# Kernel tuning notes

Hardware: AMD Instinct MI355X
Metric: run time of the kernel (lower is better)

The kernel has to match this reference:

```python
import jax, jax.numpy as jnp
import numpy as np

B, N, D, E, C, R = 4, 4096, 2048, 8, 2, 128
K = N * C // E  # tokens routed to each adapter (capacity) = 1024


def setup_inputs() -> dict:
    key = jax.random.key(0)
    ks = jax.random.split(key, 6)
    sc = lambda k, shape, s: (jax.random.normal(k, shape, jnp.float32) * s)
    return {
        "x": sc(ks[0], (B, N, D), 1.0),
        "residual": sc(ks[1], (B, N, D), 1.0),
        "Wg": sc(ks[2], (D, E), 1.0 / np.sqrt(D)),
        "bg": jnp.zeros((E,), jnp.float32),
        "Wd": sc(ks[3], (E, D, R), 1.0 / np.sqrt(D)),
        "bd": jnp.zeros((E, R), jnp.float32),
        "Wu": sc(ks[4], (E, R, D), 1.0 / np.sqrt(R)),
        "bu": jnp.zeros((E, D), jnp.float32),
    }


def reference(x, residual, Wg, bg, Wd, bd, Wu, bu):
    # Gate logits. NOTE: the original code's `nn.Softmax(X).dim` IS the raw
    # logits tensor, so top-k runs on UN-softmaxed logits (faithful quirk).
    logits = x @ Wg + bg                                   # [B,N,E]
    G, I = jax.lax.top_k(jnp.swapaxes(logits, 1, 2), K)    # [B,E,K] each

    # Dispatch: gather top-k tokens per adapter (== one-hot einsum in source).
    X_in = jnp.take_along_axis(x[:, None, :, :], I[..., None], axis=2)  # [B,E,K,D]

    # Per-adapter bottleneck MLP with residual (Adapter: up(relu(down(x))) + x).
    h = jax.nn.relu(jnp.einsum('bekd,edr->bekr', X_in, Wd) + bd[None, :, None, :])
    up = jnp.einsum('bekr,erd->bekd', h, Wu) + bu[None, :, None, :]
    X_e = up + X_in                                        # [B,E,K,D]

    # Weighted scatter-combine back to token positions (== one-hot einsum).
    contrib = (G[..., None] * X_e).reshape(B, E * K, D)
    idx = I.reshape(B, E * K)
    combine = jax.vmap(lambda i, v: jnp.zeros((N, D), x.dtype).at[i].add(v))(idx, contrib)
    return combine + residual
```

## Files before the change

kernel.cpp:

```cpp
#include <hip/hip_runtime.h>

#define B_ 4
#define N_ 4096
#define D_ 2048
#define E_ 8
#define R_ 128
#define K_ 1024

typedef __attribute__((ext_vector_type(8))) short bf16x8;
typedef __attribute__((ext_vector_type(4))) float f32x4;

__device__ inline unsigned short f2bf(float f) {
  unsigned u = __float_as_uint(f);
  unsigned r = (u + 0x7FFFu + ((u >> 16) & 1u)) >> 16;
  return (unsigned short)r;
}

__global__ __launch_bounds__(1024) void gate_kernel(const float* __restrict__ x,
                                                    const float* __restrict__ Wg,
                                                    const float* __restrict__ bg,
                                                    float* __restrict__ logitsT,
                                                    unsigned short* __restrict__ xbf) {
  __shared__ float sWg[E_ * D_];
  int tid = threadIdx.x;
  for (int f = tid * 4; f < D_ * E_; f += 1024 * 4) {
    float4 w = *(const float4*)(Wg + f);
    int d = f >> 3, e0 = f & 7;
    sWg[(e0 + 0) * D_ + d] = w.x;
    sWg[(e0 + 1) * D_ + d] = w.y;
    sWg[(e0 + 2) * D_ + d] = w.z;
    sWg[(e0 + 3) * D_ + d] = w.w;
  }
  __syncthreads();

  int wave = tid >> 6;
  int lane = tid & 63;
  int token = blockIdx.x * 16 + wave;
  int b = token >> 12;
  int n = token & (N_ - 1);
  const float* xr = x + (size_t)token * D_;
  unsigned short* xbr = xbf + (size_t)token * D_;
  float acc[E_];
#pragma unroll
  for (int e = 0; e < E_; ++e) acc[e] = 0.f;
  for (int d0 = lane * 4; d0 < D_; d0 += 256) {
    float4 xv = *(const float4*)(xr + d0);
    ushort4 o;
    o.x = f2bf(xv.x); o.y = f2bf(xv.y); o.z = f2bf(xv.z); o.w = f2bf(xv.w);
    *(ushort4*)(xbr + d0) = o;
#pragma unroll
    for (int e = 0; e < E_; ++e) {
      float4 w = *(const float4*)(&sWg[e * D_ + d0]);
      acc[e] += xv.x * w.x + xv.y * w.y + xv.z * w.z + xv.w * w.w;
    }
  }
#pragma unroll
  for (int off = 32; off > 0; off >>= 1) {
#pragma unroll
    for (int e = 0; e < E_; ++e) acc[e] += __shfl_down(acc[e], off, 64);
  }
  if (lane == 0) {
#pragma unroll
    for (int e = 0; e < E_; ++e)
      logitsT[((size_t)b * E_ + e) * N_ + n] = acc[e] + bg[e];
  }
}

__global__ __launch_bounds__(1024) void topk_kernel(const float* __restrict__ logitsT,
                                                    int* __restrict__ I,
                                                    float* __restrict__ G) {
  __shared__ unsigned keys[N_];
  __shared__ unsigned hist[256];
  __shared__ int candA[N_];
  __shared__ int candB[N_];
  __shared__ unsigned s_cnt;
  __shared__ unsigned s_prefix;
  __shared__ int s_rem;

  int be = blockIdx.x;
  const float* lg = logitsT + (size_t)be * N_;
  int tid = threadIdx.x;

  for (int n = tid; n < N_; n += 1024) {
    unsigned u = __float_as_uint(lg[n]);
    keys[n] = (u & 0x80000000u) ? ~u : (u | 0x80000000u);
  }
  if (tid < 256) hist[tid] = 0;
  if (tid == 0) s_cnt = 0;
  __syncthreads();

  for (int n = tid; n < N_; n += 1024) atomicAdd(&hist[keys[n] >> 24], 1u);
  __syncthreads();
  if (tid == 0) {
    int r = K_;
    int d = 255;
    for (; d > 0; --d) {
      int c = (int)hist[d];
      if (c >= r) break;
      r -= c;
    }
    s_prefix = (unsigned)d << 24;
    s_rem = r;
  }
  __syncthreads();
  {
    unsigned pfx = s_prefix;
    for (int n = tid; n < N_; n += 1024)
      if ((keys[n] & 0xFF000000u) == pfx) candA[atomicAdd(&s_cnt, 1u)] = n;
  }
  __syncthreads();
  int nc = (int)s_cnt;

  int* cur = candA;
  int* nxt = candB;
#pragma unroll
  for (int pass = 1; pass < 4; ++pass) {
    int shift = 24 - 8 * pass;
    __syncthreads();
    if (tid < 256) hist[tid] = 0;
    if (tid == 0) s_cnt = 0;
    __syncthreads();
    for (int i = tid; i < nc; i += 1024)
      atomicAdd(&hist[(keys[cur[i]] >> shift) & 255u], 1u);
    __syncthreads();
    if (tid == 0) {
      int r = s_rem;
      int d = 255;
      for (; d > 0; --d) {
        int c = (int)hist[d];
        if (c >= r) break;
        r -= c;
      }
      s_prefix |= (unsigned)d << shift;
      s_rem = r;
    }
    __syncthreads();
    {
      unsigned want = s_prefix;
      unsigned msk = 0xFFFFFFFFu << shift;
      for (int i = tid; i < nc; i += 1024) {
        int n = cur[i];
        if ((keys[n] & msk) == want) nxt[atomicAdd(&s_cnt, 1u)] = n;
      }
    }
    __syncthreads();
    nc = (int)s_cnt;
    int* t = cur; cur = nxt; nxt = t;
  }

  unsigned kth = s_prefix;
  int rem = s_rem;
  int nties = nc;
  __syncthreads();
  if (tid == 0) s_cnt = 0;
  __syncthreads();

  int* Ibe = I + (size_t)be * K_;
  float* Gbe = G + (size_t)be * K_;
  for (int n = tid; n < N_; n += 1024) {
    unsigned k = keys[n];
    if (k > kth) {
      unsigned p = atomicAdd(&s_cnt, 1u);
      unsigned u = (k & 0x80000000u) ? (k ^ 0x80000000u) : ~k;
      Ibe[p] = n;
      Gbe[p] = __uint_as_float(u);
    }
  }
  int base = K_ - rem;
  unsigned uk = (kth & 0x80000000u) ? (kth ^ 0x80000000u) : ~kth;
  float tieval = __uint_as_float(uk);
  for (int i = tid; i < nties; i += 1024) {
    int n = cur[i];
    int rank = 0;
    for (int j = 0; j < nties; ++j) rank += (cur[j] < n) ? 1 : 0;
    if (rank < rem) {
      Ibe[base + rank] = n;
      Gbe[base + rank] = tieval;
    }
  }
}

__global__ __launch_bounds__(256) void cvt_wd_kernel(const float* __restrict__ Wd,
                                                     unsigned short* __restrict__ WdT) {
  int t = blockIdx.x * 256 + threadIdx.x;
  int d = t & (D_ - 1);
  int r = (t >> 11) & (R_ - 1);
  int e = t >> 18;
  WdT[t] = f2bf(Wd[((size_t)e * D_ + d) * R_ + r]);
}

__global__ __launch_bounds__(256) void cvt_wu_kernel(const float* __restrict__ Wu,
                                                     unsigned short* __restrict__ WuT) {
  int t = blockIdx.x * 256 + threadIdx.x;
  int r = t & (R_ - 1);
  int d = (t >> 7) & (D_ - 1);
  int e = t >> 18;
  WuT[t] = f2bf(Wu[((size_t)e * R_ + r) * D_ + d]);
}

__global__ __launch_bounds__(256) void init_out_kernel(const float4* __restrict__ res,
                                                       float4* __restrict__ out, int n4) {
  int i = blockIdx.x * blockDim.x + threadIdx.x;
  if (i < n4) out[i] = res[i];
}

__global__ __launch_bounds__(256) void down_mfma(const unsigned short* __restrict__ xbf,
                                                 const unsigned short* __restrict__ WdT,
                                                 const float* __restrict__ bd,
                                                 const int* __restrict__ I,
                                                 unsigned short* __restrict__ h) {
  __shared__ unsigned short As[64 * 72] __attribute__((aligned(16)));
  __shared__ unsigned short Bs[128 * 72] __attribute__((aligned(16)));
  __shared__ int s_tok[64];
  int be = blockIdx.x;
  int m0 = blockIdx.y * 64;
  int b = be >> 3, e = be & 7;
  int tid = threadIdx.x;
  if (tid < 64) s_tok[tid] = I[be * K_ + m0 + tid];
  __syncthreads();
  int lane = tid & 63, wave = tid >> 6;
  int l15 = lane & 15, quad = lane >> 4;
  int wrow = (wave >> 1) * 32, wcol = (wave & 1) * 64;

  const unsigned short* srcA[2];
  int dstA[2];
#pragma unroll
  for (int i = 0; i < 2; ++i) {
    int g = tid + 256 * i;
    int row = g >> 3, part = g & 7;
    srcA[i] = xbf + ((size_t)(b * N_ + s_tok[row])) * D_ + part * 8;
    dstA[i] = row * 72 + part * 8;
  }
  const unsigned short* Wde = WdT + (size_t)e * R_ * D_;
  const unsigned short* srcB[4];
  int dstB[4];
#pragma unroll
  for (int i = 0; i < 4; ++i) {
    int g = tid + 256 * i;
    int row = g >> 3, part = g & 7;
    srcB[i] = Wde + (size_t)row * D_ + part * 8;
    dstB[i] = row * 72 + part * 8;
  }

  f32x4 zv = {0.f, 0.f, 0.f, 0.f};
  f32x4 acc[2][4];
#pragma unroll
  for (int mi = 0; mi < 2; ++mi)
#pragma unroll
    for (int ni = 0; ni < 4; ++ni) acc[mi][ni] = zv;

  for (int d0 = 0; d0 < D_; d0 += 64) {
#pragma unroll
    for (int i = 0; i < 2; ++i)
      *(uint4*)&As[dstA[i]] = *(const uint4*)(srcA[i] + d0);
#pragma unroll
    for (int i = 0; i < 4; ++i)
      *(uint4*)&Bs[dstB[i]] = *(const uint4*)(srcB[i] + d0);
    __syncthreads();
#pragma unroll
    for (int ks = 0; ks < 64; ks += 32) {
      bf16x8 a[2], bb[4];
#pragma unroll
      for (int mi = 0; mi < 2; ++mi)
        a[mi] = *(const bf16x8*)&As[(wrow + mi * 16 + l15) * 72 + ks + quad * 8];
#pragma unroll
      for (int ni = 0; ni < 4; ++ni)
        bb[ni] = *(const bf16x8*)&Bs[(wcol + ni * 16 + l15) * 72 + ks + quad * 8];
#pragma unroll
      for (int mi = 0; mi < 2; ++mi)
#pragma unroll
        for (int ni = 0; ni < 4; ++ni)
          acc[mi][ni] = __builtin_amdgcn_mfma_f32_16x16x32_bf16(a[mi], bb[ni], acc[mi][ni], 0, 0, 0);
    }
    __syncthreads();
  }
#pragma unroll
  for (int mi = 0; mi < 2; ++mi) {
#pragma unroll
    for (int ni = 0; ni < 4; ++ni) {
      int col = wcol + ni * 16 + l15;
      float bias = bd[e * R_ + col];
#pragma unroll
      for (int r = 0; r < 4; ++r) {
        int mrow = m0 + wrow + mi * 16 + quad * 4 + r;
        float v = acc[mi][ni][r] + bias;
        h[((size_t)be * K_ + mrow) * R_ + col] = f2bf(v > 0.f ? v : 0.f);
      }
    }
  }
}

__global__ __launch_bounds__(256) void up_mfma(const float* __restrict__ x,
                                               const unsigned short* __restrict__ WuT,
                                               const float* __restrict__ bu,
                                               const int* __restrict__ I,
                                               const float* __restrict__ G,
                                               const unsigned short* __restrict__ h,
                                               float* __restrict__ out, int e) {
  __shared__ unsigned short As[128 * 136] __attribute__((aligned(16)));
  __shared__ unsigned short Bs[128 * 136] __attribute__((aligned(16)));
  __shared__ int s_tok[128];
  __shared__ float s_g[128];
  int ntile = blockIdx.x;
  int mtile = blockIdx.y;
  int b = blockIdx.z;
  int be = b * E_ + e;
  int m0 = mtile * 128, n0 = ntile * 128;
  int tid = threadIdx.x;
  if (tid < 128) {
    s_tok[tid] = I[be * K_ + m0 + tid];
    s_g[tid] = G[be * K_ + m0 + tid];
  }
  const unsigned short* hbe = h + ((size_t)be * K_ + m0) * R_;
  const unsigned short* Wue = WuT + ((size_t)e * D_ + n0) * R_;
#pragma unroll
  for (int i = 0; i < 8; ++i) {
    int g = tid + 256 * i;
    int row = g >> 4, part = g & 15;
    *(uint4*)&As[row * 136 + part * 8] = *(const uint4*)(hbe + (size_t)row * R_ + part * 8);
  }
#pragma unroll
  for (int i = 0; i < 8; ++i) {
    int g = tid + 256 * i;
    int row = g >> 4, part = g & 15;
    *(uint4*)&Bs[row * 136 + part * 8] = *(const uint4*)(Wue + (size_t)row * R_ + part * 8);
  }
  __syncthreads();

  int lane = tid & 63, wave = tid >> 6;
  int l15 = lane & 15, quad = lane >> 4;
  int wrow = (wave >> 1) * 64, wcol = (wave & 1) * 64;
  f32x4 zv = {0.f, 0.f, 0.f, 0.f};
  f32x4 acc[4][4];
#pragma unroll
  for (int mi = 0; mi < 4; ++mi)
#pragma unroll
    for (int ni = 0; ni < 4; ++ni) acc[mi][ni] = zv;

#pragma unroll
  for (int ks = 0; ks < 128; ks += 32) {
    bf16x8 a[4], bb[4];
#pragma unroll
    for (int mi = 0; mi < 4; ++mi)
      a[mi] = *(const bf16x8*)&As[(wrow + mi * 16 + l15) * 136 + ks + quad * 8];
#pragma unroll
    for (int ni = 0; ni < 4; ++ni)
      bb[ni] = *(const bf16x8*)&Bs[(wcol + ni * 16 + l15) * 136 + ks + quad * 8];
#pragma unroll
    for (int mi = 0; mi < 4; ++mi)
#pragma unroll
      for (int ni = 0; ni < 4; ++ni)
        acc[mi][ni] = __builtin_amdgcn_mfma_f32_16x16x32_bf16(a[mi], bb[ni], acc[mi][ni], 0, 0, 0);
  }

#pragma unroll
  for (int mi = 0; mi < 4; ++mi) {
#pragma unroll
    for (int r = 0; r < 4; ++r) {
      int row = wrow + mi * 16 + quad * 4 + r;
      int tok = s_tok[row];
      float g = s_g[row];
      const float* xr = x + ((size_t)(b * N_ + tok)) * D_ + n0;
      float* outr = out + ((size_t)(b * N_ + tok)) * D_ + n0;
#pragma unroll
      for (int ni = 0; ni < 4; ++ni) {
        int col = wcol + ni * 16 + l15;
        float v = g * (acc[mi][ni][r] + bu[e * D_ + n0 + col] + xr[col]);
        outr[col] += v;
      }
    }
  }
}

extern "C" void kernel_launch(void* const* d_in, const int* in_sizes, int n_in,
                              void* d_out, int out_size, void* d_ws, size_t ws_size,
                              hipStream_t stream) {
  const float* x        = (const float*)d_in[0];
  const float* residual = (const float*)d_in[1];
  const float* Wg       = (const float*)d_in[2];
  const float* bg       = (const float*)d_in[3];
  const float* Wd       = (const float*)d_in[4];
  const float* bd       = (const float*)d_in[5];
  const float* Wu       = (const float*)d_in[6];
  const float* bu       = (const float*)d_in[7];
  float* out = (float*)d_out;

  char* p = (char*)d_ws;
  float* logitsT = (float*)p;            p += (size_t)B_ * E_ * N_ * 4;
  int* Ibuf = (int*)p;                   p += (size_t)B_ * E_ * K_ * 4;
  float* Gbuf = (float*)p;               p += (size_t)B_ * E_ * K_ * 4;
  unsigned short* xbf = (unsigned short*)p;  p += (size_t)B_ * N_ * D_ * 2;
  unsigned short* WdT = (unsigned short*)p;  p += (size_t)E_ * R_ * D_ * 2;
  unsigned short* WuT = (unsigned short*)p;  p += (size_t)E_ * D_ * R_ * 2;
  unsigned short* hbuf = (unsigned short*)p;

  gate_kernel<<<B_ * N_ / 16, 1024, 0, stream>>>(x, Wg, bg, logitsT, xbf);
  topk_kernel<<<B_ * E_, 1024, 0, stream>>>(logitsT, Ibuf, Gbuf);
  cvt_wd_kernel<<<E_ * D_ * R_ / 256, 256, 0, stream>>>(Wd, WdT);
  cvt_wu_kernel<<<E_ * D_ * R_ / 256, 256, 0, stream>>>(Wu, WuT);
  init_out_kernel<<<B_ * N_ * D_ / 4 / 256, 256, 0, stream>>>(
      (const float4*)residual, (float4*)out, B_ * N_ * D_ / 4);
  down_mfma<<<dim3(B_ * E_, K_ / 64), 256, 0, stream>>>(xbf, WdT, bd, Ibuf, hbuf);
  for (int e = 0; e < E_; ++e)
    up_mfma<<<dim3(D_ / 128, K_ / 128, B_), 256, 0, stream>>>(
        x, WuT, bu, Ibuf, Gbuf, hbuf, out, e);
}
```

Before: 633.7 us.

## Replace per-expert scatter-add with inverse index and gather-combine kernel

Builds an inverse token-to-expert-slot map with atomics, runs the up projection for all experts in a single launch writing dense per-expert outputs, and then combines them per token in a gather kernel that also adds the residual and the gated input. This removes eight serialized launches with read-modify-write scatter into the output, as well as the separate residual copy. In exchange it adds a large intermediate buffer that must be written and read back, and the order of the combine sum depends on atomic slot assignment.

```diff
diff --git a/kernel.cpp b/kernel.cpp
--- a/kernel.cpp
+++ b/kernel.cpp
@@ -198,10 +198,25 @@
   WuT[t] = f2bf(Wu[((size_t)e * R_ + r) * D_ + d]);
 }
 
-__global__ __launch_bounds__(256) void init_out_kernel(const float4* __restrict__ res,
-                                                       float4* __restrict__ out, int n4) {
-  int i = blockIdx.x * blockDim.x + threadIdx.x;
-  if (i < n4) out[i] = res[i];
+__global__ __launch_bounds__(256) void zero_cnt_kernel(int* __restrict__ cnt) {
+  int i = blockIdx.x * 256 + threadIdx.x;
+  if (i < B_ * N_) cnt[i] = 0;
+}
+
+__global__ __launch_bounds__(256) void build_inv_kernel(const int* __restrict__ I,
+                                                        const float* __restrict__ G,
+                                                        int* __restrict__ cnt,
+                                                        int* __restrict__ entI,
+                                                        float* __restrict__ entG) {
+  int idx = blockIdx.x * 256 + threadIdx.x;
+  int be = idx >> 10;
+  int k = idx & (K_ - 1);
+  int b = be >> 3, e = be & 7;
+  int tok = I[idx];
+  float g = G[idx];
+  int slot = atomicAdd(&cnt[b * N_ + tok], 1);
+  entI[(b * N_ + tok) * E_ + slot] = (e << 16) | k;
+  entG[(b * N_ + tok) * E_ + slot] = g;
 }
 
 __global__ __launch_bounds__(256) void down_mfma(const unsigned short* __restrict__ xbf,
@@ -290,27 +305,18 @@
   }
 }
 
-__global__ __launch_bounds__(256) void up_mfma(const float* __restrict__ x,
-                                               const unsigned short* __restrict__ WuT,
-                                               const float* __restrict__ bu,
-                                               const int* __restrict__ I,
-                                               const float* __restrict__ G,
-                                               const unsigned short* __restrict__ h,
-                                               float* __restrict__ out, int e) {
+__global__ __launch_bounds__(256) void up_all_mfma(const unsigned short* __restrict__ WuT,
+                                                   const float* __restrict__ bu,
+                                                   const unsigned short* __restrict__ h,
+                                                   float* __restrict__ contrib) {
   __shared__ unsigned short As[128 * 136] __attribute__((aligned(16)));
   __shared__ unsigned short Bs[128 * 136] __attribute__((aligned(16)));
-  __shared__ int s_tok[128];
-  __shared__ float s_g[128];
   int ntile = blockIdx.x;
   int mtile = blockIdx.y;
-  int b = blockIdx.z;
-  int be = b * E_ + e;
+  int be = blockIdx.z;
+  int e = be & 7;
   int m0 = mtile * 128, n0 = ntile * 128;
   int tid = threadIdx.x;
-  if (tid < 128) {
-    s_tok[tid] = I[be * K_ + m0 + tid];
-    s_g[tid] = G[be * K_ + m0 + tid];
-  }
   const unsigned short* hbe = h + ((size_t)be * K_ + m0) * R_;
   const unsigned short* Wue = WuT + ((size_t)e * D_ + n0) * R_;
 #pragma unroll
@@ -358,18 +364,67 @@
 #pragma unroll
     for (int r = 0; r < 4; ++r) {
       int row = wrow + mi * 16 + quad * 4 + r;
-      int tok = s_tok[row];
-      float g = s_g[row];
-      const float* xr = x + ((size_t)(b * N_ + tok)) * D_ + n0;
-      float* outr = out + ((size_t)(b * N_ + tok)) * D_ + n0;
+      float* outr = contrib + ((size_t)be * K_ + m0 + row) * D_ + n0;
 #pragma unroll
       for (int ni = 0; ni < 4; ++ni) {
         int col = wcol + ni * 16 + l15;
-        float v = g * (acc[mi][ni][r] + bu[e * D_ + n0 + col] + xr[col]);
-        outr[col] += v;
+        outr[col] = acc[mi][ni][r] + bu[e * D_ + n0 + col];
       }
     }
   }
+}
+
+__global__ __launch_bounds__(256) void combine_kernel(const float* __restrict__ x,
+                                                      const float* __restrict__ residual,
+                                                      const float* __restrict__ contrib,
+                                                      const int* __restrict__ cnt,
+                                                      const int* __restrict__ entI,
+                                                      const float* __restrict__ entG,
+                                                      float* __restrict__ out) {
+  __shared__ int s_c;
+  __shared__ int s_ei[E_];
+  __shared__ float s_gv[E_];
+  int bn = blockIdx.x;
+  int tid = threadIdx.x;
+  if (tid == 0) s_c = cnt[bn];
+  if (tid < E_) {
+    s_ei[tid] = entI[bn * E_ + tid];
+    s_gv[tid] = entG[bn * E_ + tid];
+  }
+  __syncthreads();
+  int c = s_c;
+
+  size_t rowoff = (size_t)bn * D_ + tid * 8;
+  float4 r0 = *(const float4*)(residual + rowoff);
+  float4 r1 = *(const float4*)(residual + rowoff + 4);
+  float4 xv0 = *(const float4*)(x + rowoff);
+  float4 xv1 = *(const float4*)(x + rowoff + 4);
+
+  float s = 0.f;
+  float4 a0 = {0.f, 0.f, 0.f, 0.f}, a1 = {0.f, 0.f, 0.f, 0.f};
+  int b = bn >> 12;
+  for (int i = 0; i < c; ++i) {
+    int ei = s_ei[i];
+    float g = s_gv[i];
+    s += g;
+    int e = ei >> 16, k = ei & 0xFFFF;
+    const float* cr = contrib + ((size_t)(b * E_ + e) * K_ + k) * D_ + tid * 8;
+    float4 c0 = *(const float4*)(cr);
+    float4 c1 = *(const float4*)(cr + 4);
+    a0.x += g * c0.x; a0.y += g * c0.y; a0.z += g * c0.z; a0.w += g * c0.w;
+    a1.x += g * c1.x; a1.y += g * c1.y; a1.z += g * c1.z; a1.w += g * c1.w;
+  }
+  float4 o0, o1;
+  o0.x = r0.x + s * xv0.x + a0.x;
+  o0.y = r0.y + s * xv0.y + a0.y;
+  o0.z = r0.z + s * xv0.z + a0.z;
+  o0.w = r0.w + s * xv0.w + a0.w;
+  o1.x = r1.x + s * xv1.x + a1.x;
+  o1.y = r1.y + s * xv1.y + a1.y;
+  o1.z = r1.z + s * xv1.z + a1.z;
+  o1.w = r1.w + s * xv1.w + a1.w;
+  *(float4*)(out + rowoff) = o0;
+  *(float4*)(out + rowoff + 4) = o1;
 }
 
 extern "C" void kernel_launch(void* const* d_in, const int* in_sizes, int n_in,
@@ -392,16 +447,19 @@
   unsigned short* xbf = (unsigned short*)p;  p += (size_t)B_ * N_ * D_ * 2;
   unsigned short* WdT = (unsigned short*)p;  p += (size_t)E_ * R_ * D_ * 2;
   unsigned short* WuT = (unsigned short*)p;  p += (size_t)E_ * D_ * R_ * 2;
-  unsigned short* hbuf = (unsigned short*)p;
+  unsigned short* hbuf = (unsigned short*)p; p += (size_t)B_ * E_ * K_ * R_ * 2;
+  int* cnt = (int*)p;                    p += (size_t)B_ * N_ * 4;
+  int* entI = (int*)p;                   p += (size_t)B_ * N_ * E_ * 4;
+  float* entG = (float*)p;               p += (size_t)B_ * N_ * E_ * 4;
+  float* contrib = (float*)p;
 
   gate_kernel<<<B_ * N_ / 16, 1024, 0, stream>>>(x, Wg, bg, logitsT, xbf);
   topk_kernel<<<B_ * E_, 1024, 0, stream>>>(logitsT, Ibuf, Gbuf);
   cvt_wd_kernel<<<E_ * D_ * R_ / 256, 256, 0, stream>>>(Wd, WdT);
   cvt_wu_kernel<<<E_ * D_ * R_ / 256, 256, 0, stream>>>(Wu, WuT);
-  init_out_kernel<<<B_ * N_ * D_ / 4 / 256, 256, 0, stream>>>(
-      (const float4*)residual, (float4*)out, B_ * N_ * D_ / 4);
+  zero_cnt_kernel<<<(B_ * N_ + 255) / 256, 256, 0, stream>>>(cnt);
+  build_inv_kernel<<<B_ * E_ * K_ / 256, 256, 0, stream>>>(Ibuf, Gbuf, cnt, entI, entG);
   down_mfma<<<dim3(B_ * E_, K_ / 64), 256, 0, stream>>>(xbf, WdT, bd, Ibuf, hbuf);
-  for (int e = 0; e < E_; ++e)
-    up_mfma<<<dim3(D_ / 128, K_ / 128, B_), 256, 0, stream>>>(
-        x, WuT, bu, Ibuf, Gbuf, hbuf, out, e);
-}
+  up_all_mfma<<<dim3(D_ / 128, K_ / 128, B_ * E_), 256, 0, stream>>>(WuT, bu, hbuf, contrib);
+  combine_kernel<<<B_ * N_, 256, 0, stream>>>(x, residual, contrib, cnt, entI, entG, out);
+}
```

Result: faster. 593.8 us (-6.3%).
